# Kernel optimization log

Measured on AMD Instinct MI355X. Metric: run time of the kernel, lower is better.

The kernel has to match this reference:

```python
import jax, jax.numpy as jnp
import numpy as np

N = 50000
E = 800000
EPS = 1e-16
NEG_SLOPE = 0.2

def setup_inputs() -> dict:
    key = jax.random.key(0)
    ks = jax.random.split(key, 10)
    s = lambda fan: 1.0 / np.sqrt(fan)
    return {
        "x": jax.random.normal(ks[0], (N, 128), dtype=jnp.float32),
        "edge_index": jax.random.randint(ks[1], (2, E), 0, N, dtype=jnp.int64),
        "W1": jax.random.normal(ks[2], (128, 4 * 32), dtype=jnp.float32) * s(128),
        "att_src1": jax.random.normal(ks[3], (4, 32), dtype=jnp.float32) * s(32),
        "att_dst1": jax.random.normal(ks[4], (4, 32), dtype=jnp.float32) * s(32),
        "b1": jnp.zeros((128,), dtype=jnp.float32),
        "W2": jax.random.normal(ks[5], (128, 2), dtype=jnp.float32) * s(128),
        "att_src2": jax.random.normal(ks[6], (1, 2), dtype=jnp.float32) * s(2),
        "att_dst2": jax.random.normal(ks[7], (1, 2), dtype=jnp.float32) * s(2),
        "b2": jnp.zeros((2,), dtype=jnp.float32),
    }

def _gat_conv(x, src, dst, W, att_src, att_dst, bias, heads, out_ch, concat):
    n = x.shape[0]
    h = (x @ W).reshape(n, heads, out_ch)                      # [N,H,C]
    a_src = jnp.sum(h * att_src[None], axis=-1)                # [N,H]
    a_dst = jnp.sum(h * att_dst[None], axis=-1)                # [N,H]
    e = jax.nn.leaky_relu(a_src[src] + a_dst[dst], NEG_SLOPE)  # [Etot,H]
    # segment softmax over incoming edges per destination node
    m = jax.ops.segment_max(e, dst, num_segments=n)            # [N,H]
    m = jnp.where(jnp.isfinite(m), m, 0.0)
    ex = jnp.exp(e - m[dst])
    denom = jax.ops.segment_sum(ex, dst, num_segments=n)       # [N,H]
    alpha = ex / (denom[dst] + EPS)                            # [Etot,H]
    out = jax.ops.segment_sum(alpha[:, :, None] * h[src], dst, num_segments=n)  # [N,H,C]
    if concat:
        out = out.reshape(n, heads * out_ch)
    else:
        out = out.mean(axis=1)
    return out + bias

def reference(x, edge_index, W1, att_src1, att_dst1, b1, W2, att_src2, att_dst2, b2):
    n = x.shape[0]
    # PyG GATConv adds self-loops by default
    loops = jnp.arange(n, dtype=edge_index.dtype)
    src = jnp.concatenate([edge_index[0], loops])
    dst = jnp.concatenate([edge_index[1], loops])
    # dropout is identity at inference
    h = jax.nn.elu(_gat_conv(x, src, dst, W1, att_src1, att_dst1, b1, 4, 32, True))
    h = _gat_conv(h, src, dst, W2, att_src2, att_dst2, b2, 1, 2, False)
    return jax.nn.log_softmax(h, axis=1)
```

## Files before the change

### kernel.cpp

```cpp
#include <hip/hip_runtime.h>
#include <hip/hip_bf16.h>

#define NN 50000
#define EE 800000
#define CAP 64
#define NEG_SLOPE 0.2f
#define EPSF 1e-16f
#define BUILD_BLOCKS 4096
#define GEMM_BLOCKS ((NN + 63) / 64)
#define POISON_BASE ((int)0xAAAAAAAAu)
#define LDSROW 136

typedef unsigned int uint32;
typedef unsigned short u16;
typedef __attribute__((ext_vector_type(8))) short short8;
typedef __attribute__((ext_vector_type(4))) float floatx4;

__device__ __forceinline__ u16 f2bf(float f) {
  unsigned int u = __float_as_uint(f);
  unsigned int r = (u + 0x7fffu + ((u >> 16) & 1u)) >> 16;
  return (u16)r;
}
__device__ __forceinline__ float bf_lo(uint32 v) { return __uint_as_float(v << 16); }
__device__ __forceinline__ float bf_hi(uint32 v) { return __uint_as_float(v & 0xffff0000u); }
__device__ __forceinline__ float lrelu(float e) { return (e > 0.f) ? e : NEG_SLOPE * e; }

__device__ __forceinline__ void do_build(int b, int nb, const int* __restrict__ ei,
                                         int* __restrict__ counts,
                                         u16* __restrict__ csr) {
  const int range = b & 7;
  const int lo = range * (NN / 8);
  const int hi = lo + (NN / 8);
  const int group = b >> 3;
  const int ngr = nb >> 3;
  const int4* __restrict__ dst4 = (const int4*)(ei + EE);
  const int4* __restrict__ src4 = (const int4*)ei;
  for (int c = group * 256 + threadIdx.x; c < EE / 4; c += ngr * 256) {
    int4 d = dst4[c];
    int4 s = src4[c];
    if (d.x >= lo && d.x < hi) {
      int r = atomicAdd(&counts[d.x], 1) - POISON_BASE;
      if (r < CAP) csr[d.x * CAP + r] = (u16)s.x;
    }
    if (d.y >= lo && d.y < hi) {
      int r = atomicAdd(&counts[d.y], 1) - POISON_BASE;
      if (r < CAP) csr[d.y * CAP + r] = (u16)s.y;
    }
    if (d.z >= lo && d.z < hi) {
      int r = atomicAdd(&counts[d.z], 1) - POISON_BASE;
      if (r < CAP) csr[d.z * CAP + r] = (u16)s.z;
    }
    if (d.w >= lo && d.w < hi) {
      int r = atomicAdd(&counts[d.w], 1) - POISON_BASE;
      if (r < CAP) csr[d.w * CAP + r] = (u16)s.w;
    }
  }
}

__global__ __launch_bounds__(256) void work_k(
    const int* __restrict__ ei, int* __restrict__ counts, u16* __restrict__ csr,
    const float* __restrict__ x, const float* __restrict__ W1,
    const float* __restrict__ att_src1, const float* __restrict__ att_dst1,
    uint32* __restrict__ h1b, float* __restrict__ as1, float* __restrict__ ad1) {
  __shared__ u16 WtL[128 * LDSROW];

  const int b = blockIdx.x;
  const int t = threadIdx.x;

  if (b < BUILD_BLOCKS) {
    do_build(b, BUILD_BLOCKS, ei, counts, csr);
    return;
  }

  #pragma unroll
  for (int i = 0; i < 16; i++) {
    int v = t + i * 256;
    int k = v >> 5, c4 = v & 31;
    float4 w = *(const float4*)&W1[k * 128 + c4 * 4];
    WtL[(c4 * 4 + 0) * LDSROW + k] = f2bf(w.x);
    WtL[(c4 * 4 + 1) * LDSROW + k] = f2bf(w.y);
    WtL[(c4 * 4 + 2) * LDSROW + k] = f2bf(w.z);
    WtL[(c4 * 4 + 3) * LDSROW + k] = f2bf(w.w);
  }
  __syncthreads();

  const int tile = b - BUILD_BLOCKS;
  const int wave = t >> 6;
  const int lane = t & 63;
  const int quad = lane >> 4;
  const int col  = lane & 15;
  const int nodeBase = tile * 64 + wave * 16;

  floatx4 acc[8];
  #pragma unroll
  for (int i = 0; i < 8; i++) acc[i] = (floatx4){0.f, 0.f, 0.f, 0.f};

  int mread = nodeBase + col; if (mread >= NN) mread = NN - 1;
  const float* __restrict__ xrow = x + (size_t)mread * 128 + quad * 8;

  #pragma unroll
  for (int ks = 0; ks < 4; ks++) {
    float4 a0 = *(const float4*)(xrow + ks * 32);
    float4 a1 = *(const float4*)(xrow + ks * 32 + 4);
    union { short8 v; u16 u[8]; } af;
    af.u[0] = f2bf(a0.x); af.u[1] = f2bf(a0.y);
    af.u[2] = f2bf(a0.z); af.u[3] = f2bf(a0.w);
    af.u[4] = f2bf(a1.x); af.u[5] = f2bf(a1.y);
    af.u[6] = f2bf(a1.z); af.u[7] = f2bf(a1.w);
    #pragma unroll
    for (int tt = 0; tt < 8; tt++) {
      short8 bf = *(const short8*)&WtL[(tt * 16 + col) * LDSROW + ks * 32 + quad * 8];
      acc[tt] = __builtin_amdgcn_mfma_f32_16x16x32_bf16(af.v, bf, acc[tt], 0, 0, 0);
    }
  }

  float asv[8], adv[8];
  #pragma unroll
  for (int tt = 0; tt < 8; tt++) {
    asv[tt] = att_src1[tt * 16 + col];
    adv[tt] = att_dst1[tt * 16 + col];
  }

  #pragma unroll
  for (int r = 0; r < 4; r++) {
    const int gn = nodeBase + quad * 4 + r;
    const bool live = (gn < NN);
    #pragma unroll
    for (int tt = 0; tt < 8; tt++) {
      float v = acc[tt][r];
      float w = __shfl_xor(v, 1, 64);
      if (live && ((col & 1) == 0)) {
        uint32 pk = (uint32)f2bf(v) | ((uint32)f2bf(w) << 16);
        h1b[(size_t)gn * 64 + tt * 8 + (col >> 1)] = pk;
      }
    }
    #pragma unroll
    for (int h = 0; h < 4; h++) {
      float ps = acc[2 * h][r] * asv[2 * h] + acc[2 * h + 1][r] * asv[2 * h + 1];
      float pd = acc[2 * h][r] * adv[2 * h] + acc[2 * h + 1][r] * adv[2 * h + 1];
      #pragma unroll
      for (int off = 1; off < 16; off <<= 1) {
        ps += __shfl_xor(ps, off, 64);
        pd += __shfl_xor(pd, off, 64);
      }
      if (live && col == 0) {
        as1[gn * 4 + h] = ps;
        ad1[gn * 4 + h] = pd;
      }
    }
  }
}

__global__ __launch_bounds__(256) void agg1_k(
    const int* __restrict__ counts, const u16* __restrict__ csr,
    const uint32* __restrict__ h1b, const float* __restrict__ as1,
    const float* __restrict__ ad1, const float* __restrict__ b1,
    const float* __restrict__ W2, const float* __restrict__ att_src2,
    const float* __restrict__ att_dst2,
    float* __restrict__ h2, float* __restrict__ as2, float* __restrict__ ad2) {
  const int lane = threadIdx.x & 63;
  const int n = __builtin_amdgcn_readfirstlane(blockIdx.x * 4 + (threadIdx.x >> 6));
  const int hd = lane >> 4;

  int cnt = __builtin_amdgcn_readfirstlane(counts[n]) - POISON_BASE;
  cnt = (cnt < CAP) ? cnt : CAP;
  const u16* __restrict__ row = csr + n * CAP;
  const float adv = ad1[n * 4 + hd];

  float xs = __expf(lrelu(as1[n * 4 + hd] + adv));
  uint32 vs = h1b[n * 64 + lane];
  float den = xs;
  float accx = xs * bf_lo(vs), accy = xs * bf_hi(vs);

  int j = 0;
  for (; j + 7 < cnt; j += 8) {
    union { uint4 v; u16 u[8]; } ss;
    ss.v = *(const uint4*)(row + j);
    int s[8];
    #pragma unroll
    for (int q = 0; q < 8; q++) s[q] = ss.u[q];
    float e[8];
    #pragma unroll
    for (int q = 0; q < 8; q++) e[q] = as1[s[q] * 4 + hd];
    uint32 v[8];
    #pragma unroll
    for (int q = 0; q < 8; q++) v[q] = h1b[s[q] * 64 + lane];
    #pragma unroll
    for (int q = 0; q < 8; q++) {
      float ex = __expf(lrelu(e[q] + adv));
      den += ex;
      accx = fmaf(ex, bf_lo(v[q]), accx);
      accy = fmaf(ex, bf_hi(v[q]), accy);
    }
  }
  for (; j < cnt; j++) {
    int s = row[j];
    float ex = __expf(lrelu(as1[s * 4 + hd] + adv));
    uint32 v = h1b[s * 64 + lane];
    den += ex;
    accx = fmaf(ex, bf_lo(v), accx);
    accy = fmaf(ex, bf_hi(v), accy);
  }

  float inv = 1.f / (den + EPSF);
  float2 bb = ((const float2*)b1)[lane];
  float ox = accx * inv + bb.x;
  float oy = accy * inv + bb.y;
  ox = (ox > 0.f) ? ox : (__expf(ox) - 1.f);
  oy = (oy > 0.f) ? oy : (__expf(oy) - 1.f);

  float4 wq = ((const float4*)W2)[lane];
  float p0 = ox * wq.x + oy * wq.z;
  float p1 = ox * wq.y + oy * wq.w;
  #pragma unroll
  for (int off = 32; off; off >>= 1) {
    p0 += __shfl_xor(p0, off, 64);
    p1 += __shfl_xor(p1, off, 64);
  }
  if (lane == 0) {
    *(float2*)&h2[n * 2] = make_float2(p0, p1);
    as2[n] = p0 * att_src2[0] + p1 * att_src2[1];
    ad2[n] = p0 * att_dst2[0] + p1 * att_dst2[1];
  }
}

__global__ __launch_bounds__(256) void agg2_k(
    const int* __restrict__ counts, const u16* __restrict__ csr,
    const float* __restrict__ h2, const float* __restrict__ as2,
    const float* __restrict__ ad2, const float* __restrict__ b2,
    float* __restrict__ out) {
  int i = blockIdx.x * 256 + threadIdx.x;
  if (i >= NN * 8) return;
  int n = i >> 3;
  int sub = i & 7;
  const float adv = ad2[n];
  int cnt = counts[n] - POISON_BASE;
  cnt = (cnt < CAP) ? cnt : CAP;
  const u16* __restrict__ row = csr + n * CAP;
  const float2* __restrict__ h2v = (const float2*)h2;

  float den = 0.f, a0 = 0.f, a1 = 0.f;
  if (sub == 0) {
    float xs = __expf(lrelu(as2[n] + adv));
    float2 hv = h2v[n];
    den = xs; a0 = xs * hv.x; a1 = xs * hv.y;
  }
  for (int j = sub; j < cnt; j += 8) {
    int s = row[j];
    float ex = __expf(lrelu(as2[s] + adv));
    float2 hv = h2v[s];
    den += ex;
    a0 = fmaf(ex, hv.x, a0);
    a1 = fmaf(ex, hv.y, a1);
  }
  #pragma unroll
  for (int off = 4; off; off >>= 1) {
    den += __shfl_down(den, off, 8);
    a0  += __shfl_down(a0, off, 8);
    a1  += __shfl_down(a1, off, 8);
  }
  if (sub == 0) {
    float inv = 1.f / (den + EPSF);
    float o0 = a0 * inv + b2[0];
    float o1 = a1 * inv + b2[1];
    float mx = fmaxf(o0, o1);
    float lse = mx + __logf(__expf(o0 - mx) + __expf(o1 - mx));
    *(float2*)&out[n * 2] = make_float2(o0 - lse, o1 - lse);
  }
}

extern "C" void kernel_launch(void* const* d_in, const int* in_sizes, int n_in,
                              void* d_out, int out_size, void* d_ws, size_t ws_size,
                              hipStream_t stream) {
  const float* x        = (const float*)d_in[0];
  const int*   ei       = (const int*)d_in[1];
  const float* W1       = (const float*)d_in[2];
  const float* att_src1 = (const float*)d_in[3];
  const float* att_dst1 = (const float*)d_in[4];
  const float* b1       = (const float*)d_in[5];
  const float* W2       = (const float*)d_in[6];
  const float* att_src2 = (const float*)d_in[7];
  const float* att_dst2 = (const float*)d_in[8];
  const float* b2       = (const float*)d_in[9];
  float* out = (float*)d_out;

  char* p = (char*)d_ws;
  auto alloc = [&](size_t bytes) {
    char* r = p;
    p += (bytes + 255) & ~size_t(255);
    return r;
  };
  uint32* h1b  = (uint32*)alloc(sizeof(uint32) * NN * 64);
  float* as1   = (float*)alloc(sizeof(float) * NN * 4);
  float* ad1   = (float*)alloc(sizeof(float) * NN * 4);
  float* h2    = (float*)alloc(sizeof(float) * NN * 2);
  float* as2   = (float*)alloc(sizeof(float) * NN);
  float* ad2   = (float*)alloc(sizeof(float) * NN);
  int*   counts = (int*)alloc(sizeof(int) * NN);
  u16*   csr   = (u16*)alloc(sizeof(u16) * NN * CAP);

  work_k<<<BUILD_BLOCKS + GEMM_BLOCKS, 256, 0, stream>>>(
      ei, counts, csr, x, W1, att_src1, att_dst1, h1b, as1, ad1);
  agg1_k<<<NN / 4, 256, 0, stream>>>(counts, csr, h1b, as1, ad1, b1, W2,
                                     att_src2, att_dst2, h2, as2, ad2);
  agg2_k<<<(NN * 8 + 255) / 256, 256, 0, stream>>>(counts, csr, h2, as2, ad2,
                                                   b2, out);
}
```

Measured before the change: 196.6 us.

## Bin CSR edges in shared memory per node range before global flush

The CSR build blocks now each own a 448-node range and a quarter of the edge list. They count and bin source indices with LDS atomics, then flush each node's bin to global memory with one global atomicAdd per node. The goal is to replace about 800k scattered global atomics with far fewer global atomics plus mostly-local work. In exchange, each block now scans a larger slice of dst and reloads src with scalar reads. The per-range local capacity of 32 could silently drop edges for unusually high-degree nodes within a chunk.

```diff
diff --git a/kernel.cpp b/kernel.cpp
--- a/kernel.cpp
+++ b/kernel.cpp
@@ -6,10 +6,16 @@
 #define CAP 64
 #define NEG_SLOPE 0.2f
 #define EPSF 1e-16f
-#define BUILD_BLOCKS 4096
-#define GEMM_BLOCKS ((NN + 63) / 64)
 #define POISON_BASE ((int)0xAAAAAAAAu)
 #define LDSROW 136
+
+#define NPB 448
+#define NRANGE 112
+#define SCHUNK 4
+#define BUILD_BLOCKS (NRANGE * SCHUNK)
+#define CLCAP 32
+#define CQ (EE / 4 / SCHUNK)
+#define GEMM_BLOCKS ((NN + 63) / 64)
 
 typedef unsigned int uint32;
 typedef unsigned short u16;
@@ -24,54 +30,67 @@
 __device__ __forceinline__ float bf_lo(uint32 v) { return __uint_as_float(v << 16); }
 __device__ __forceinline__ float bf_hi(uint32 v) { return __uint_as_float(v & 0xffff0000u); }
 __device__ __forceinline__ float lrelu(float e) { return (e > 0.f) ? e : NEG_SLOPE * e; }
-
-__device__ __forceinline__ void do_build(int b, int nb, const int* __restrict__ ei,
-                                         int* __restrict__ counts,
-                                         u16* __restrict__ csr) {
-  const int range = b & 7;
-  const int lo = range * (NN / 8);
-  const int hi = lo + (NN / 8);
-  const int group = b >> 3;
-  const int ngr = nb >> 3;
-  const int4* __restrict__ dst4 = (const int4*)(ei + EE);
-  const int4* __restrict__ src4 = (const int4*)ei;
-  for (int c = group * 256 + threadIdx.x; c < EE / 4; c += ngr * 256) {
-    int4 d = dst4[c];
-    int4 s = src4[c];
-    if (d.x >= lo && d.x < hi) {
-      int r = atomicAdd(&counts[d.x], 1) - POISON_BASE;
-      if (r < CAP) csr[d.x * CAP + r] = (u16)s.x;
-    }
-    if (d.y >= lo && d.y < hi) {
-      int r = atomicAdd(&counts[d.y], 1) - POISON_BASE;
-      if (r < CAP) csr[d.y * CAP + r] = (u16)s.y;
-    }
-    if (d.z >= lo && d.z < hi) {
-      int r = atomicAdd(&counts[d.z], 1) - POISON_BASE;
-      if (r < CAP) csr[d.z * CAP + r] = (u16)s.z;
-    }
-    if (d.w >= lo && d.w < hi) {
-      int r = atomicAdd(&counts[d.w], 1) - POISON_BASE;
-      if (r < CAP) csr[d.w * CAP + r] = (u16)s.w;
-    }
-  }
-}
 
 __global__ __launch_bounds__(256) void work_k(
     const int* __restrict__ ei, int* __restrict__ counts, u16* __restrict__ csr,
     const float* __restrict__ x, const float* __restrict__ W1,
     const float* __restrict__ att_src1, const float* __restrict__ att_dst1,
     uint32* __restrict__ h1b, float* __restrict__ as1, float* __restrict__ ad1) {
-  __shared__ u16 WtL[128 * LDSROW];
+  __shared__ u16 smem[128 * LDSROW];
 
   const int b = blockIdx.x;
   const int t = threadIdx.x;
 
   if (b < BUILD_BLOCKS) {
-    do_build(b, BUILD_BLOCKS, ei, counts, csr);
+    u16* __restrict__ bins = smem;
+    int* __restrict__ cnt  = (int*)(smem + NPB * CLCAP);
+    const int r  = b % NRANGE;
+    const int sc = b / NRANGE;
+    const int lo = r * NPB;
+    const int nloc = (lo + NPB <= NN) ? NPB : (NN - lo);
+    const int hi = lo + nloc;
+
+    for (int i = t; i < nloc; i += 256) cnt[i] = 0;
+    __syncthreads();
+
+    const int4* __restrict__ dst4 = (const int4*)(ei + EE);
+    const int c0 = sc * CQ, c1 = c0 + CQ;
+    for (int c = c0 + t; c < c1; c += 256) {
+      int4 d = dst4[c];
+      if (d.x >= lo && d.x < hi) {
+        int rl = atomicAdd(&cnt[d.x - lo], 1);
+        if (rl < CLCAP) bins[(d.x - lo) * CLCAP + rl] = (u16)ei[c * 4 + 0];
+      }
+      if (d.y >= lo && d.y < hi) {
+        int rl = atomicAdd(&cnt[d.y - lo], 1);
+        if (rl < CLCAP) bins[(d.y - lo) * CLCAP + rl] = (u16)ei[c * 4 + 1];
+      }
+      if (d.z >= lo && d.z < hi) {
+        int rl = atomicAdd(&cnt[d.z - lo], 1);
+        if (rl < CLCAP) bins[(d.z - lo) * CLCAP + rl] = (u16)ei[c * 4 + 2];
+      }
+      if (d.w >= lo && d.w < hi) {
+        int rl = atomicAdd(&cnt[d.w - lo], 1);
+        if (rl < CLCAP) bins[(d.w - lo) * CLCAP + rl] = (u16)ei[c * 4 + 3];
+      }
+    }
+    __syncthreads();
+
+    for (int i = t; i < nloc; i += 256) {
+      int c = cnt[i]; if (c > CLCAP) c = CLCAP;
+      if (c > 0) {
+        int n = lo + i;
+        int base = atomicAdd(&counts[n], c) - POISON_BASE;
+        u16* __restrict__ dstp = csr + (size_t)n * CAP;
+        #pragma unroll 4
+        for (int k = 0; k < c; k++)
+          if (base + k < CAP) dstp[base + k] = bins[i * CLCAP + k];
+      }
+    }
     return;
   }
 
+  u16* __restrict__ WtL = smem;
   #pragma unroll
   for (int i = 0; i < 16; i++) {
     int v = t + i * 256;
```

New measurement: 281.0 us. +43.0%, slower.

## Split layer-1 neighbor aggregation of each node across two wavefronts

Applied to the files above, without the earlier changes.

The first-layer aggregation kernel now assigns two wavefronts per destination node, each handling alternating 8-edge chunks of the neighbor list. Partial sums are combined through shared memory before the epilogue. The intent is to shorten each wave's serial gather latency chain and increase memory-level parallelism for low-degree nodes. In exchange it doubles the wave count, adds LDS traffic and a block barrier, and leaves half the waves idle during the epilogue.

```diff
diff --git a/kernel.cpp b/kernel.cpp
--- a/kernel.cpp
+++ b/kernel.cpp
@@ -158,8 +158,14 @@
     const float* __restrict__ W2, const float* __restrict__ att_src2,
     const float* __restrict__ att_dst2,
     float* __restrict__ h2, float* __restrict__ as2, float* __restrict__ ad2) {
-  const int lane = threadIdx.x & 63;
-  const int n = __builtin_amdgcn_readfirstlane(blockIdx.x * 4 + (threadIdx.x >> 6));
+  __shared__ float pden[2][64], pax[2][64], pay[2][64];
+
+  const int t = threadIdx.x;
+  const int lane = t & 63;
+  const int wv = t >> 6;
+  const int slot = wv >> 1;
+  const int half = wv & 1;
+  const int n = __builtin_amdgcn_readfirstlane(blockIdx.x * 2 + slot);
   const int hd = lane >> 4;
 
   int cnt = __builtin_amdgcn_readfirstlane(counts[n]) - POISON_BASE;
@@ -167,40 +173,60 @@
   const u16* __restrict__ row = csr + n * CAP;
   const float adv = ad1[n * 4 + hd];
 
-  float xs = __expf(lrelu(as1[n * 4 + hd] + adv));
-  uint32 vs = h1b[n * 64 + lane];
-  float den = xs;
-  float accx = xs * bf_lo(vs), accy = xs * bf_hi(vs);
-
-  int j = 0;
-  for (; j + 7 < cnt; j += 8) {
-    union { uint4 v; u16 u[8]; } ss;
-    ss.v = *(const uint4*)(row + j);
-    int s[8];
-    #pragma unroll
-    for (int q = 0; q < 8; q++) s[q] = ss.u[q];
-    float e[8];
-    #pragma unroll
-    for (int q = 0; q < 8; q++) e[q] = as1[s[q] * 4 + hd];
-    uint32 v[8];
-    #pragma unroll
-    for (int q = 0; q < 8; q++) v[q] = h1b[s[q] * 64 + lane];
-    #pragma unroll
-    for (int q = 0; q < 8; q++) {
-      float ex = __expf(lrelu(e[q] + adv));
-      den += ex;
-      accx = fmaf(ex, bf_lo(v[q]), accx);
-      accy = fmaf(ex, bf_hi(v[q]), accy);
-    }
-  }
-  for (; j < cnt; j++) {
-    int s = row[j];
-    float ex = __expf(lrelu(as1[s * 4 + hd] + adv));
-    uint32 v = h1b[s * 64 + lane];
-    den += ex;
-    accx = fmaf(ex, bf_lo(v), accx);
-    accy = fmaf(ex, bf_hi(v), accy);
-  }
+  float den = 0.f, accx = 0.f, accy = 0.f;
+  if (half == 0) {
+    float xs = __expf(lrelu(as1[n * 4 + hd] + adv));
+    uint32 vs = h1b[(size_t)n * 64 + lane];
+    den = xs;
+    accx = xs * bf_lo(vs);
+    accy = xs * bf_hi(vs);
+  }
+
+  const int nch = (cnt + 7) >> 3;
+  for (int c = half; c < nch; c += 2) {
+    const int base = c * 8;
+    int m = cnt - base; m = (m > 8) ? 8 : m;
+    if (m == 8) {
+      union { uint4 v; u16 u[8]; } ss;
+      ss.v = *(const uint4*)(row + base);
+      int s[8];
+      #pragma unroll
+      for (int q = 0; q < 8; q++) s[q] = ss.u[q];
+      float e[8];
+      #pragma unroll
+      for (int q = 0; q < 8; q++) e[q] = as1[s[q] * 4 + hd];
+      uint32 v[8];
+      #pragma unroll
+      for (int q = 0; q < 8; q++) v[q] = h1b[(size_t)s[q] * 64 + lane];
+      #pragma unroll
+      for (int q = 0; q < 8; q++) {
+        float ex = __expf(lrelu(e[q] + adv));
+        den += ex;
+        accx = fmaf(ex, bf_lo(v[q]), accx);
+        accy = fmaf(ex, bf_hi(v[q]), accy);
+      }
+    } else {
+      for (int k = 0; k < m; k++) {
+        int s = row[base + k];
+        float ex = __expf(lrelu(as1[s * 4 + hd] + adv));
+        uint32 v = h1b[(size_t)s * 64 + lane];
+        den += ex;
+        accx = fmaf(ex, bf_lo(v), accx);
+        accy = fmaf(ex, bf_hi(v), accy);
+      }
+    }
+  }
+
+  if (half == 1) {
+    pden[slot][lane] = den;
+    pax[slot][lane] = accx;
+    pay[slot][lane] = accy;
+  }
+  __syncthreads();
+  if (half == 1) return;
+  den  += pden[slot][lane];
+  accx += pax[slot][lane];
+  accy += pay[slot][lane];
 
   float inv = 1.f / (den + EPSF);
   float2 bb = ((const float2*)b1)[lane];
@@ -301,7 +327,7 @@
 
   work_k<<<BUILD_BLOCKS + GEMM_BLOCKS, 256, 0, stream>>>(
       ei, counts, csr, x, W1, att_src1, att_dst1, h1b, as1, ad1);
-  agg1_k<<<NN / 4, 256, 0, stream>>>(counts, csr, h1b, as1, ad1, b1, W2,
+  agg1_k<<<NN / 2, 256, 0, stream>>>(counts, csr, h1b, as1, ad1, b1, W2,
                                      att_src2, att_dst2, h2, as2, ad2);
   agg2_k<<<(NN * 8 + 255) / 256, 256, 0, stream>>>(counts, csr, h2, as2, ad2,
                                                    b2, out);
```

After: 215.4 us. 9.6% more time.

## Precompute per-edge attention exponentials in a separate kernel before aggregation

Applied to the files above, without the earlier changes.

Adds a kernel that computes exp(leaky_relu(a_src+a_dst)) for every CSR slot and all four heads, and stores the results as float4 in a padded per-node buffer. The layer-1 aggregation then reads these precomputed weights instead of gathering as1 by source index and evaluating exp per lane. The aim is to take the dependent gather and transcendental work off the aggregation's critical path. In exchange it adds a kernel launch and a 51 MB buffer that must be written and read back through memory.

```diff
diff --git a/kernel.cpp b/kernel.cpp
--- a/kernel.cpp
+++ b/kernel.cpp
@@ -151,8 +151,31 @@
   }
 }
 
+__global__ __launch_bounds__(256) void ew_k(
+    const int* __restrict__ counts, const u16* __restrict__ csr,
+    const float* __restrict__ as1, const float* __restrict__ ad1,
+    float4* __restrict__ exw) {
+  int i = blockIdx.x * 256 + threadIdx.x;
+  if (i >= NN * CAP) return;
+  int n = i >> 6;
+  int j = i & (CAP - 1);
+  int cnt = counts[n] - POISON_BASE;
+  cnt = (cnt < CAP) ? cnt : CAP;
+  if (j >= cnt) return;
+  int s = csr[i];
+  float4 a = ((const float4*)as1)[s];
+  float4 d = ((const float4*)ad1)[n];
+  float4 r;
+  r.x = __expf(lrelu(a.x + d.x));
+  r.y = __expf(lrelu(a.y + d.y));
+  r.z = __expf(lrelu(a.z + d.z));
+  r.w = __expf(lrelu(a.w + d.w));
+  exw[i] = r;
+}
+
 __global__ __launch_bounds__(256) void agg1_k(
     const int* __restrict__ counts, const u16* __restrict__ csr,
+    const float* __restrict__ exwf,
     const uint32* __restrict__ h1b, const float* __restrict__ as1,
     const float* __restrict__ ad1, const float* __restrict__ b1,
     const float* __restrict__ W2, const float* __restrict__ att_src2,
@@ -165,10 +188,10 @@
   int cnt = __builtin_amdgcn_readfirstlane(counts[n]) - POISON_BASE;
   cnt = (cnt < CAP) ? cnt : CAP;
   const u16* __restrict__ row = csr + n * CAP;
-  const float adv = ad1[n * 4 + hd];
-
-  float xs = __expf(lrelu(as1[n * 4 + hd] + adv));
-  uint32 vs = h1b[n * 64 + lane];
+  const float* __restrict__ ew = exwf + (size_t)n * CAP * 4 + hd;
+
+  float xs = __expf(lrelu(as1[n * 4 + hd] + ad1[n * 4 + hd]));
+  uint32 vs = h1b[(size_t)n * 64 + lane];
   float den = xs;
   float accx = xs * bf_lo(vs), accy = xs * bf_hi(vs);
 
@@ -176,30 +199,26 @@
   for (; j + 7 < cnt; j += 8) {
     union { uint4 v; u16 u[8]; } ss;
     ss.v = *(const uint4*)(row + j);
-    int s[8];
-    #pragma unroll
-    for (int q = 0; q < 8; q++) s[q] = ss.u[q];
     float e[8];
     #pragma unroll
-    for (int q = 0; q < 8; q++) e[q] = as1[s[q] * 4 + hd];
+    for (int q = 0; q < 8; q++) e[q] = ew[(j + q) * 4];
     uint32 v[8];
     #pragma unroll
-    for (int q = 0; q < 8; q++) v[q] = h1b[s[q] * 64 + lane];
+    for (int q = 0; q < 8; q++) v[q] = h1b[(size_t)ss.u[q] * 64 + lane];
     #pragma unroll
     for (int q = 0; q < 8; q++) {
-      float ex = __expf(lrelu(e[q] + adv));
-      den += ex;
-      accx = fmaf(ex, bf_lo(v[q]), accx);
-      accy = fmaf(ex, bf_hi(v[q]), accy);
+      den += e[q];
+      accx = fmaf(e[q], bf_lo(v[q]), accx);
+      accy = fmaf(e[q], bf_hi(v[q]), accy);
     }
   }
   for (; j < cnt; j++) {
     int s = row[j];
-    float ex = __expf(lrelu(as1[s * 4 + hd] + adv));
-    uint32 v = h1b[s * 64 + lane];
-    den += ex;
-    accx = fmaf(ex, bf_lo(v), accx);
-    accy = fmaf(ex, bf_hi(v), accy);
+    float e = ew[j * 4];
+    uint32 v = h1b[(size_t)s * 64 + lane];
+    den += e;
+    accx = fmaf(e, bf_lo(v), accx);
+    accy = fmaf(e, bf_hi(v), accy);
   }
 
   float inv = 1.f / (den + EPSF);
@@ -298,11 +317,13 @@
   float* ad2   = (float*)alloc(sizeof(float) * NN);
   int*   counts = (int*)alloc(sizeof(int) * NN);
   u16*   csr   = (u16*)alloc(sizeof(u16) * NN * CAP);
+  float4* exw  = (float4*)alloc(sizeof(float4) * NN * CAP);
 
   work_k<<<BUILD_BLOCKS + GEMM_BLOCKS, 256, 0, stream>>>(
       ei, counts, csr, x, W1, att_src1, att_dst1, h1b, as1, ad1);
-  agg1_k<<<NN / 4, 256, 0, stream>>>(counts, csr, h1b, as1, ad1, b1, W2,
-                                     att_src2, att_dst2, h2, as2, ad2);
+  ew_k<<<(NN * CAP) / 256, 256, 0, stream>>>(counts, csr, as1, ad1, exw);
+  agg1_k<<<NN / 4, 256, 0, stream>>>(counts, csr, (const float*)exw, h1b, as1,
+                                     ad1, b1, W2, att_src2, att_dst2, h2, as2, ad2);
   agg2_k<<<(NN * 8 + 255) / 256, 256, 0, stream>>>(counts, csr, h2, as2, ad2,
                                                    b2, out);
 }
```

New measurement: 205.6 us. +4.6%, slower.
